# Kernel tuning notes

Measured on AMD Instinct MI355X. Metric: run time of the kernel, lower is better.

The kernel has to match this reference:

```python
import jax, jax.numpy as jnp
import numpy as np

B, T, C, H = 2, 2048, 1024, 16
D = C // H  # head dim = 64
EPS = 1e-5


def _layernorm(x, g, b):
    mu = jnp.mean(x, axis=-1, keepdims=True)
    var = jnp.mean((x - mu) ** 2, axis=-1, keepdims=True)
    return (x - mu) * jax.lax.rsqrt(var + EPS) * g + b


def setup_inputs() -> dict:
    key = jax.random.key(0)
    ks = jax.random.split(key, 16)
    s = 1.0 / np.sqrt(C)
    inp = {
        "x": jax.random.normal(ks[0], (B, T, C), dtype=jnp.float32),
        "Wq": jax.random.normal(ks[1], (C, C), dtype=jnp.float32) * s,
        "bq": jnp.zeros((C,), jnp.float32),
        "Wk": jax.random.normal(ks[2], (C, C), dtype=jnp.float32) * s,
        "bk": jnp.zeros((C,), jnp.float32),
        "Wv": jax.random.normal(ks[3], (C, C), dtype=jnp.float32) * s,
        "bv": jnp.zeros((C,), jnp.float32),
        "Wo": jax.random.normal(ks[4], (C, C), dtype=jnp.float32) * s,
        "bo": jnp.zeros((C,), jnp.float32),
        "ln1_g": jnp.ones((C,), jnp.float32),
        "ln1_b": jnp.zeros((C,), jnp.float32),
        "ln2_g": jnp.ones((C,), jnp.float32),
        "ln2_b": jnp.zeros((C,), jnp.float32),
        "W1": jax.random.normal(ks[5], (C, 4 * C), dtype=jnp.float32) * s,
        "b1": jnp.zeros((4 * C,), jnp.float32),
        "W2": jax.random.normal(ks[6], (4 * C, C), dtype=jnp.float32) * (1.0 / np.sqrt(4 * C)),
        "b2": jnp.zeros((C,), jnp.float32),
    }
    return inp


def _block(x, Wq, bq, Wk, bk, Wv, bv, Wo, bo, ln1_g, ln1_b, ln2_g, ln2_b, W1, b1, W2, b2):
    # --- attention sublayer (pre-LN, residual) ---
    h = _layernorm(x, ln1_g, ln1_b)
    q = (h @ Wq + bq).reshape(B, T, H, D)
    k = (h @ Wk + bk).reshape(B, T, H, D)
    v = (h @ Wv + bv).reshape(B, T, H, D)
    scores = jnp.einsum("bthd,bshd->bhts", q, k) * (1.0 / np.sqrt(D))
    attn = jax.nn.softmax(scores, axis=-1)  # dropout is identity at eval
    y = jnp.einsum("bhts,bshd->bthd", attn, v).reshape(B, T, C)
    x = x + (y @ Wo + bo)
    # --- MLP sublayer (pre-LN, residual) ---
    h2 = _layernorm(x, ln2_g, ln2_b)
    m = jax.nn.gelu(h2 @ W1 + b1, approximate=False)  # torch nn.GELU() is exact erf
    x = x + (m @ W2 + b2)
    return x


def reference(x, Wq, bq, Wk, bk, Wv, bv, Wo, bo, ln1_g, ln1_b, ln2_g, ln2_b, W1, b1, W2, b2):
    return _block(x, Wq, bq, Wk, bk, Wv, bv, Wo, bo, ln1_g, ln1_b, ln2_g, ln2_b, W1, b1, W2, b2)
```

## Files before the change

### kernel.cpp

```cpp
#include <hip/hip_runtime.h>
#include <math.h>

typedef unsigned short u16;
typedef unsigned int   u32;
using bf16x8 = __attribute__((ext_vector_type(8))) short;
using f32x4  = __attribute__((ext_vector_type(4))) float;
using f32x16 = __attribute__((ext_vector_type(16))) float;

static constexpr int Bb = 2, Tt = 2048, Cc = 1024, Hh = 16, Dd = 64;
static constexpr int QS = 3072;
static constexpr float QSCALE = 0.125f * 1.44269504089f;

__device__ __forceinline__ u16 f2bf(float f){
  u32 u = __builtin_bit_cast(u32, f);
  u += 0x7fffu + ((u >> 16) & 1u);
  return (u16)(u >> 16);
}
__device__ __forceinline__ float bf2f(u16 v){
  u32 u = (u32)v << 16;
  return __builtin_bit_cast(float, u);
}

__device__ __forceinline__ void gl2lds16(const void* g, void* l){
  __builtin_amdgcn_global_load_lds((const __attribute__((address_space(1))) void*)g,
                                   (__attribute__((address_space(3))) void*)l, 16, 0, 0);
}

template<int N> __device__ __forceinline__ void waitvm(){
  if constexpr (N == 0) asm volatile("s_waitcnt vmcnt(0)" ::: "memory");
  else if constexpr (N == 4) asm volatile("s_waitcnt vmcnt(4)" ::: "memory");
  else if constexpr (N == 6) asm volatile("s_waitcnt vmcnt(6)" ::: "memory");
  else if constexpr (N == 8) asm volatile("s_waitcnt vmcnt(8)" ::: "memory");
}

__device__ __forceinline__ void barrier_pin(){
  __builtin_amdgcn_s_barrier();
  __builtin_amdgcn_sched_barrier(0);
}

__device__ __forceinline__ f32x4 mfma16(bf16x8 a, bf16x8 b, f32x4 c){
  return __builtin_amdgcn_mfma_f32_16x16x32_bf16(a, b, c, 0, 0, 0);
}
__device__ __forceinline__ f32x16 mfma32(bf16x8 a, bf16x8 b, f32x16 c){
  return __builtin_amdgcn_mfma_f32_32x32x16_bf16(a, b, c, 0, 0, 0);
}

__device__ __forceinline__ float exp2f_fast(float x){
#if __has_builtin(__builtin_amdgcn_exp2f)
  return __builtin_amdgcn_exp2f(x);
#else
  return __expf(x * 0.69314718056f);
#endif
}

__device__ __forceinline__ float gelu_f(float x){
  return 0.5f * x * (1.0f + erff(x * 0.70710678118654752f));
}

__device__ __forceinline__ void plane_swap(u32& a, u32& b){
  asm("v_permlane32_swap_b32 %0, %1" : "+v"(a), "+v"(b));
}
__device__ __forceinline__ u32 cvtpk_bf16(float lo, float hi){
  u32 r;
  asm("v_cvt_pk_bf16_f32 %0, %1, %2" : "=v"(r) : "v"(lo), "v"(hi));
  return r;
}

__device__ __forceinline__ bf16x8 ldlds(const u16* p){ return *(const bf16x8*)p; }

__global__ __launch_bounds__(256) void ln_kernel(const float* __restrict__ x,
    const float* __restrict__ g, const float* __restrict__ b, u16* __restrict__ out)
{
  int row = blockIdx.x;
  int tid = threadIdx.x;
  const float4* xr = (const float4*)(x + (size_t)row * Cc);
  float4 v = xr[tid];
  float s  = v.x + v.y + v.z + v.w;
  float s2 = v.x*v.x + v.y*v.y + v.z*v.z + v.w*v.w;
  #pragma unroll
  for (int off = 1; off < 64; off <<= 1){ s += __shfl_xor(s, off); s2 += __shfl_xor(s2, off); }
  __shared__ float red[8];
  int wid = tid >> 6;
  if ((tid & 63) == 0){ red[wid] = s; red[4 + wid] = s2; }
  __syncthreads();
  s  = red[0] + red[1] + red[2] + red[3];
  s2 = red[4] + red[5] + red[6] + red[7];
  float mu   = s * (1.0f / Cc);
  float var  = s2 * (1.0f / Cc) - mu * mu;
  float rstd = rsqrtf(var + 1e-5f);
  const float4 gg = ((const float4*)g)[tid];
  const float4 bb = ((const float4*)b)[tid];
  ushort4 o;
  o.x = f2bf((v.x - mu) * rstd * gg.x + bb.x);
  o.y = f2bf((v.y - mu) * rstd * gg.y + bb.y);
  o.z = f2bf((v.z - mu) * rstd * gg.z + bb.z);
  o.w = f2bf((v.w - mu) * rstd * gg.w + bb.w);
  *(ushort4*)(out + (size_t)row * Cc + tid * 4) = o;
}

__global__ __launch_bounds__(256) void transpose_cast_kernel(const float* __restrict__ in,
    u16* __restrict__ out, int R, int Ccols)
{
  __shared__ float tile[32][33];
  int tx = threadIdx.x, ty = threadIdx.y;
  int c0 = blockIdx.x * 32, r0 = blockIdx.y * 32;
  #pragma unroll
  for (int j = 0; j < 4; j++) tile[ty + j*8][tx] = in[(size_t)(r0 + ty + j*8) * Ccols + c0 + tx];
  __syncthreads();
  #pragma unroll
  for (int j = 0; j < 4; j++) out[(size_t)(c0 + ty + j*8) * R + r0 + tx] = f2bf(tile[tx][ty + j*8]);
}

__global__ __launch_bounds__(256) void transpose4_kernel(
    const float* __restrict__ s0, const float* __restrict__ s1,
    const float* __restrict__ s2, const float* __restrict__ s3,
    u16* __restrict__ d0, u16* __restrict__ d1, u16* __restrict__ d2, u16* __restrict__ d3)
{
  __shared__ float tile[32][33];
  int z = blockIdx.z;
  const float* in = (z == 0) ? s0 : (z == 1) ? s1 : (z == 2) ? s2 : s3;
  u16* out        = (z == 0) ? d0 : (z == 1) ? d1 : (z == 2) ? d2 : d3;
  int tx = threadIdx.x, ty = threadIdx.y;
  int c0 = blockIdx.x * 32, r0 = blockIdx.y * 32;
  #pragma unroll
  for (int j = 0; j < 4; j++) tile[ty + j*8][tx] = in[(size_t)(r0 + ty + j*8) * 1024 + c0 + tx];
  __syncthreads();
  #pragma unroll
  for (int j = 0; j < 4; j++) out[(size_t)(c0 + ty + j*8) * 1024 + r0 + tx] = f2bf(tile[tx][ty + j*8]);
}

__global__ __launch_bounds__(256) void pack3_kernel(const float* __restrict__ a,
    const float* __restrict__ b, const float* __restrict__ c, float* __restrict__ o)
{
  int i = blockIdx.x * 256 + threadIdx.x;
  float v = (i < 1024) ? a[i] : (i < 2048 ? b[i - 1024] : c[i - 2048]);
  o[i] = v;
}

__global__ __launch_bounds__(256) void transpose_v_kernel(const u16* __restrict__ v, u16* __restrict__ vt)
{
  __shared__ u16 tile[32][33];
  int tx = threadIdx.x, ty = threadIdx.y;
  int bh = blockIdx.z; int b = bh >> 4, h = bh & 15;
  int t0 = blockIdx.x * 32, d0 = blockIdx.y * 32;
  const u16* src = v + (size_t)b * Tt * QS + h * Dd;
  #pragma unroll
  for (int j = 0; j < 4; j++) tile[ty + j*8][tx] = src[(size_t)(t0 + ty + j*8) * QS + d0 + tx];
  __syncthreads();
  u16* dst = vt + (size_t)bh * Dd * Tt;
  #pragma unroll
  for (int j = 0; j < 4; j++) dst[(size_t)(d0 + ty + j*8) * Tt + t0 + tx] = tile[tx][ty + j*8];
}

template<int BM, int BN, int WPEU, int EPI>
__global__ __launch_bounds__(256, WPEU) void gemmc_kernel(
    const u16* __restrict__ A, const u16* __restrict__ BT,
    const float* __restrict__ bias, const float* __restrict__ resid,
    void* __restrict__ out, int K, int ldA, int ldOut)
{
  constexpr int MF = BM / 2 / 16;
  constexpr int NF = BN / 2 / 16;
  constexpr int AG = BM / 32;
  constexpr int BG = BN / 32;
  constexpr int NLOADS = AG + BG;

  __shared__ alignas(16) u16 As[2][BM * 64];
  __shared__ alignas(16) u16 Bs[2][BN * 64];

  const int tid  = threadIdx.x;
  const int lane = tid & 63, wid = tid >> 6;
  const int l15  = lane & 15, lg = lane >> 4;

  const int gx  = gridDim.x;
  const int lin = blockIdx.x + gx * blockIdx.y;
  const int nwg = gx * gridDim.y;
  const int wl  = (lin & 7) * (nwg >> 3) + (lin >> 3);
  const int rowBase = (wl % gx) * BM, colBase = (wl / gx) * BN;

  const int wr = wid >> 1, wc = wid & 1;

  f32x4 acc[MF][NF] = {};

  const u16* pA[AG];
  const u16* pB[BG];
  u32 dA[AG], dB[BG];
  #pragma unroll
  for (int j = 0; j < AG; j++){
    int g = tid + 256 * j;
    int r = g >> 3, w = (g & 7) ^ (r & 7);
    pA[j] = A + (size_t)(rowBase + r) * ldA + w * 8;
    dA[j] = (u32)g * 8;
  }
  #pragma unroll
  for (int j = 0; j < BG; j++){
    int g = tid + 256 * j;
    int r = g >> 3, w = (g & 7) ^ (r & 7);
    pB[j] = BT + (size_t)(colBase + r) * K + w * 8;
    dB[j] = (u32)g * 8;
  }

  u32 oa[MF][2], ob[NF][2];
  #pragma unroll
  for (int mi = 0; mi < MF; mi++){
    int r = wr * (BM / 2) + mi * 16 + l15;
    oa[mi][0] = (u32)(r * 64 + ((lg       ^ (r & 7)) << 3));
    oa[mi][1] = (u32)(r * 64 + (((4 + lg) ^ (r & 7)) << 3));
  }
  #pragma unroll
  for (int ni = 0; ni < NF; ni++){
    int r = wc * (BN / 2) + ni * 16 + l15;
    ob[ni][0] = (u32)(r * 64 + ((lg       ^ (r & 7)) << 3));
    ob[ni][1] = (u32)(r * 64 + (((4 + lg) ^ (r & 7)) << 3));
  }

  #pragma unroll
  for (int j = 0; j < AG; j++){ gl2lds16(pA[j], &As[0][dA[j]]); pA[j] += 64; }
  #pragma unroll
  for (int j = 0; j < BG; j++){ gl2lds16(pB[j], &Bs[0][dB[j]]); pB[j] += 64; }

  const int nt = K >> 6;
  #pragma unroll 2
  for (int t = 0; t < nt - 1; ++t){
    const int cur = t & 1, nxt = cur ^ 1;
    #pragma unroll
    for (int j = 0; j < AG; j++){ gl2lds16(pA[j], &As[nxt][dA[j]]); pA[j] += 64; }
    #pragma unroll
    for (int j = 0; j < BG; j++){ gl2lds16(pB[j], &Bs[nxt][dB[j]]); pB[j] += 64; }
    waitvm<NLOADS>();
    __builtin_amdgcn_s_barrier();
    __builtin_amdgcn_sched_barrier(0);

    bf16x8 afr[MF][2], bfr[NF][2];
    #pragma unroll
    for (int mi = 0; mi < MF; mi++){
      afr[mi][0] = ldlds(&As[cur][oa[mi][0]]);
      afr[mi][1] = ldlds(&As[cur][oa[mi][1]]);
    }
    #pragma unroll
    for (int ni = 0; ni < NF; ni++){
      bfr[ni][0] = ldlds(&Bs[cur][ob[ni][0]]);
      bfr[ni][1] = ldlds(&Bs[cur][ob[ni][1]]);
    }
    __builtin_amdgcn_s_setprio(1);
    #pragma unroll
    for (int mi = 0; mi < MF; mi++)
      #pragma unroll
      for (int ni = 0; ni < NF; ni++){
        acc[mi][ni] = mfma16(afr[mi][0], bfr[ni][0], acc[mi][ni]);
        acc[mi][ni] = mfma16(afr[mi][1], bfr[ni][1], acc[mi][ni]);
      }
    __builtin_amdgcn_s_setprio(0);

    __builtin_amdgcn_sched_barrier(0);
    __builtin_amdgcn_s_barrier();
  }
  {
    const int cur = (nt - 1) & 1;
    waitvm<0>();
    __builtin_amdgcn_s_barrier();
    bf16x8 afr[MF][2], bfr[NF][2];
    #pragma unroll
    for (int mi = 0; mi < MF; mi++){
      afr[mi][0] = ldlds(&As[cur][oa[mi][0]]);
      afr[mi][1] = ldlds(&As[cur][oa[mi][1]]);
    }
    #pragma unroll
    for (int ni = 0; ni < NF; ni++){
      bfr[ni][0] = ldlds(&Bs[cur][ob[ni][0]]);
      bfr[ni][1] = ldlds(&Bs[cur][ob[ni][1]]);
    }
    #pragma unroll
    for (int mi = 0; mi < MF; mi++)
      #pragma unroll
      for (int ni = 0; ni < NF; ni++){
        acc[mi][ni] = mfma16(afr[mi][0], bfr[ni][0], acc[mi][ni]);
        acc[mi][ni] = mfma16(afr[mi][1], bfr[ni][1], acc[mi][ni]);
      }
  }

  #pragma unroll
  for (int mi = 0; mi < MF; mi++){
    #pragma unroll
    for (int ni = 0; ni < NF; ni++){
      int row = rowBase + wr * (BM / 2) + mi * 16 + lg * 4;
      int col = colBase + wc * (BN / 2) + ni * 16 + l15;
      float bc = bias[col];
      #pragma unroll
      for (int r = 0; r < 4; r++){
        float val = acc[mi][ni][r] + bc;
        size_t idx = (size_t)(row + r) * ldOut + col;
        if constexpr (EPI == 1)      ((float*)out)[idx] = val + resid[idx];
        else if constexpr (EPI == 2) ((u16*)out)[idx]   = f2bf(gelu_f(val));
        else if constexpr (EPI == 3) ((u16*)out)[idx]   = f2bf(col < 1024 ? val * QSCALE : val);
        else                         ((u16*)out)[idx]   = f2bf(val);
      }
    }
  }
}

__global__ __launch_bounds__(256, 4) void attn_kernel(const u16* __restrict__ q, const u16* __restrict__ k,
    const u16* __restrict__ vt, u16* __restrict__ opart, float* __restrict__ ml)
{
  __shared__ alignas(16) u16 Ks[2][64 * 64];
  __shared__ alignas(16) u16 Vs[2][64 * 64];
  int tid  = threadIdx.x;
  int lane = tid & 63, wid = tid >> 6;
  int l31  = lane & 31, hi = lane >> 5;

  int lin = blockIdx.x + 16 * blockIdx.y;
  int wl  = (lin & 7) * 64 + (lin >> 3);
  int qt  = wl & 15, bh = wl >> 4;
  int b = bh >> 4, h = bh & 15;
  int split = blockIdx.z;
  int kt0 = split * (Tt / 2);

  int qglob = qt * 128 + wid * 32 + l31;

  const u16* qp = q + ((size_t)b * Tt + qglob) * QS + h * Dd + hi * 8;
  bf16x8 qf[4];
  #pragma unroll
  for (int s = 0; s < 4; s++) qf[s] = *(const bf16x8*)(qp + s * 16);

  const u16* kbase = k  + (size_t)b * Tt * QS + h * Dd;
  const u16* vbase = vt + (size_t)bh * Dd * Tt;

  f32x16 yacc[2] = {};
  float m2 = -1e30f, lsum = 0.f;

  int g0 = tid, g1 = tid + 256;
  int r0 = g0 >> 3, cb0 = (g0 & 7) ^ (r0 & 7);
  int r1 = g1 >> 3, cb1 = (g1 & 7) ^ (r1 & 7);

  auto stageKV = [&](int buf, int kt){
    gl2lds16(kbase + (size_t)(kt + r0) * QS + cb0 * 8, (u16*)Ks[buf] + wid * 512);
    gl2lds16(kbase + (size_t)(kt + r1) * QS + cb1 * 8, (u16*)Ks[buf] + 2048 + wid * 512);
    gl2lds16(vbase + (size_t)r0 * Tt + kt + cb0 * 8,   (u16*)Vs[buf] + wid * 512);
    gl2lds16(vbase + (size_t)r1 * Tt + kt + cb1 * 8,   (u16*)Vs[buf] + 2048 + wid * 512);
  };

  stageKV(0, kt0);
  int cur = 0;
  for (int kt = kt0; kt < kt0 + Tt / 2; kt += 64) {
    if (kt + 64 < kt0 + Tt / 2) { stageKV(cur ^ 1, kt + 64); waitvm<4>(); }
    else                        { waitvm<0>(); }
    barrier_pin();

    const u16* Ksb = (const u16*)Ks[cur];
    const u16* Vsb = (const u16*)Vs[cur];
    int rx = l31 & 7;

    f32x16 st[2] = {};
    __builtin_amdgcn_s_setprio(1);
    #pragma unroll
    for (int nb = 0; nb < 2; nb++){
      const u16* krow = Ksb + (nb * 32 + l31) * 64;
      #pragma unroll
      for (int s = 0; s < 4; s++){
        bf16x8 kf = *(const bf16x8*)(krow + (((s * 2 + hi) ^ rx) << 3));
        st[nb] = mfma32(kf, qf[s], st[nb]);
      }
    }
    __builtin_amdgcn_s_setprio(0);

    float tm[16];
    #pragma unroll
    for (int i = 0; i < 16; i++) tm[i] = fmaxf(st[0][i], st[1][i]);
    #pragma unroll
    for (int w = 8; w; w >>= 1)
      #pragma unroll
      for (int i = 0; i < w; i++) tm[i] = fmaxf(tm[i], tm[i + w]);
    u32 ma = __builtin_bit_cast(u32, tm[0]), mb = ma;
    plane_swap(ma, mb);
    float mx = fmaxf(__builtin_bit_cast(float, ma), __builtin_bit_cast(float, mb));

    float mnew = fmaxf(m2, mx);
    float alpha = exp2f_fast(m2 - mnew);
    m2 = mnew;

    #pragma unroll
    for (int nb = 0; nb < 2; nb++)
      #pragma unroll
      for (int i = 0; i < 16; i++)
        st[nb][i] = exp2f_fast(st[nb][i] - m2);

    float ts[16];
    #pragma unroll
    for (int i = 0; i < 16; i++) ts[i] = st[0][i] + st[1][i];
    #pragma unroll
    for (int w = 8; w; w >>= 1)
      #pragma unroll
      for (int i = 0; i < w; i++) ts[i] += ts[i + w];
    u32 sa = __builtin_bit_cast(u32, ts[0]), sb = sa;
    plane_swap(sa, sb);
    lsum = lsum * alpha + __builtin_bit_cast(float, sa) + __builtin_bit_cast(float, sb);

    #pragma unroll
    for (int nd = 0; nd < 2; nd++)
      #pragma unroll
      for (int i = 0; i < 16; i++) yacc[nd][i] *= alpha;

    bf16x8 pb[4];
    #pragma unroll
    for (int nb = 0; nb < 2; nb++){
      u32 c[8];
      #pragma unroll
      for (int i = 0; i < 8; i++) c[i] = cvtpk_bf16(st[nb][2 * i], st[nb][2 * i + 1]);
      plane_swap(c[0], c[2]); plane_swap(c[1], c[3]);
      plane_swap(c[4], c[6]); plane_swap(c[5], c[7]);
      u32 f0[4] = {c[0], c[1], c[2], c[3]};
      u32 f1[4] = {c[4], c[5], c[6], c[7]};
      pb[nb * 2 + 0] = *(bf16x8*)f0;
      pb[nb * 2 + 1] = *(bf16x8*)f1;
    }

    __builtin_amdgcn_s_setprio(1);
    #pragma unroll
    for (int nd = 0; nd < 2; nd++){
      const u16* vrow = Vsb + (nd * 32 + l31) * 64;
      #pragma unroll
      for (int ks = 0; ks < 4; ks++){
        bf16x8 vf = *(const bf16x8*)(vrow + (((ks * 2 + hi) ^ rx) << 3));
        yacc[nd] = mfma32(vf, pb[ks], yacc[nd]);
      }
    }
    __builtin_amdgcn_s_setprio(0);

    __builtin_amdgcn_sched_barrier(0);
    barrier_pin();
    cur ^= 1;
  }

  float inv = 1.0f / lsum;
  u16* op = opart + ((size_t)split * (Bb * Tt) + (size_t)b * Tt + qglob) * Cc + h * Dd;
  #pragma unroll
  for (int nd = 0; nd < 2; nd++){
    #pragma unroll
    for (int g = 0; g < 4; g++){
      ushort4 o;
      o.x = f2bf(yacc[nd][g * 4 + 0] * inv);
      o.y = f2bf(yacc[nd][g * 4 + 1] * inv);
      o.z = f2bf(yacc[nd][g * 4 + 2] * inv);
      o.w = f2bf(yacc[nd][g * 4 + 3] * inv);
      *(ushort4*)(op + nd * 32 + g * 8 + hi * 4) = o;
    }
  }
  if (hi == 0){
    float* mlp = ml + (((size_t)split * (Bb * Tt) + (size_t)b * Tt + qglob) * Hh + h) * 2;
    mlp[0] = m2; mlp[1] = lsum;
  }
}

__global__ __launch_bounds__(256) void combine_kernel(const u16* __restrict__ opart,
    const float* __restrict__ ml, u16* __restrict__ y)
{
  int row = blockIdx.x;
  int d0  = threadIdx.x * 4;
  int h   = d0 >> 6;
  const float* p0 = ml + ((size_t)row * Hh + h) * 2;
  const float* p1 = ml + (((size_t)(Bb * Tt) + row) * Hh + h) * 2;
  float m0 = p0[0], l0 = p0[1], m1 = p1[0], l1 = p1[1];
  float M  = fmaxf(m0, m1);
  float u0 = l0 * exp2f_fast(m0 - M), u1 = l1 * exp2f_fast(m1 - M);
  float inv = 1.0f / (u0 + u1);
  float w0 = u0 * inv, w1 = u1 * inv;
  ushort4 a = *(const ushort4*)(opart + (size_t)row * Cc + d0);
  ushort4 c = *(const ushort4*)(opart + ((size_t)(Bb * Tt) + row) * Cc + d0);
  ushort4 o;
  o.x = f2bf(bf2f(a.x) * w0 + bf2f(c.x) * w1);
  o.y = f2bf(bf2f(a.y) * w0 + bf2f(c.y) * w1);
  o.z = f2bf(bf2f(a.z) * w0 + bf2f(c.z) * w1);
  o.w = f2bf(bf2f(a.w) * w0 + bf2f(c.w) * w1);
  *(ushort4*)(y + (size_t)row * Cc + d0) = o;
}

extern "C" void kernel_launch(void* const* d_in, const int* in_sizes, int n_in,
                              void* d_out, int out_size, void* d_ws, size_t ws_size,
                              hipStream_t stream)
{
  (void)in_sizes; (void)n_in; (void)out_size; (void)ws_size;
  const float* x    = (const float*)d_in[0];
  const float* Wq   = (const float*)d_in[1];
  const float* bq   = (const float*)d_in[2];
  const float* Wk   = (const float*)d_in[3];
  const float* bk   = (const float*)d_in[4];
  const float* Wv   = (const float*)d_in[5];
  const float* bv   = (const float*)d_in[6];
  const float* Wo   = (const float*)d_in[7];
  const float* bo   = (const float*)d_in[8];
  const float* ln1g = (const float*)d_in[9];
  const float* ln1b = (const float*)d_in[10];
  const float* ln2g = (const float*)d_in[11];
  const float* ln2b = (const float*)d_in[12];
  const float* W1   = (const float*)d_in[13];
  const float* b1   = (const float*)d_in[14];
  const float* W2   = (const float*)d_in[15];
  const float* b2   = (const float*)d_in[16];

  char* ws = (char*)d_ws;
  const size_t MB = 1024 * 1024;
  u16*   wqkvt = (u16*)(ws + 0 * MB);
  u16*   wot   = (u16*)(ws + 6 * MB);
  u16*   w1t   = (u16*)(ws + 8 * MB);
  u16*   w2t   = (u16*)(ws + 16 * MB);
  float* bqkv  = (float*)(ws + 24 * MB);
  u16*   hbuf  = (u16*)(ws + 25 * MB);
  u16*   qkv   = (u16*)(ws + 33 * MB);
  u16*   vtb   = (u16*)(ws + 57 * MB);
  u16*   yb    = (u16*)(ws + 65 * MB);
  u16*   opart = (u16*)(ws + 73 * MB);
  float* x2    = (float*)(ws + 73 * MB);
  float* mlb   = (float*)(ws + 89 * MB);
  u16*   h2    = hbuf;
  u16*   mb    = qkv;

  dim3 tb(32, 8);
  transpose4_kernel<<<dim3(32, 32, 4), tb, 0, stream>>>(Wq, Wk, Wv, Wo,
      wqkvt, wqkvt + 1024 * 1024, wqkvt + 2048 * 1024, wot);
  transpose_cast_kernel<<<dim3(128, 32), tb, 0, stream>>>(W1, w1t, 1024, 4096);
  transpose_cast_kernel<<<dim3(32, 128), tb, 0, stream>>>(W2, w2t, 4096, 1024);
  pack3_kernel<<<12, 256, 0, stream>>>(bq, bk, bv, bqkv);

  ln_kernel<<<4096, 256, 0, stream>>>(x, ln1g, ln1b, hbuf);

  gemmc_kernel<64, 128, 3, 3><<<dim3(64, 24), 256, 0, stream>>>(hbuf, wqkvt, bqkv, nullptr, qkv, 1024, 1024, 3072);

  transpose_v_kernel<<<dim3(64, 2, 32), tb, 0, stream>>>(qkv + 2048, vtb);

  attn_kernel<<<dim3(16, 32, 2), 256, 0, stream>>>(qkv, qkv + 1024, vtb, opart, mlb);
  combine_kernel<<<4096, 256, 0, stream>>>(opart, mlb, yb);

  gemmc_kernel<64, 64, 4, 1><<<dim3(64, 16), 256, 0, stream>>>(yb, wot, bo, x, x2, 1024, 1024, 1024);

  ln_kernel<<<4096, 256, 0, stream>>>(x2, ln2g, ln2b, h2);

  gemmc_kernel<64, 128, 3, 2><<<dim3(64, 32), 256, 0, stream>>>(h2, w1t, b1, nullptr, mb, 1024, 1024, 4096);

  gemmc_kernel<64, 64, 4, 1><<<dim3(64, 16), 256, 0, stream>>>(mb, w2t, b2, x2, (float*)d_out, 4096, 4096, 1024);
}
```

Before: 258.3 us.

## Add 256x256 eight-wave ping-pong GEMM for QKV and MLP-up projections

Adds a new 512-thread GEMM kernel with 256x256 output tiles, a split-K double-buffered LDS layout with XOR swizzle, and interleaved barriers and set-priority around MFMA phases. It replaces the smaller-tile kernel for the QKV and W1 projections. The W2 projection switches to a 128x64 tile configuration. Larger tiles cut global and LDS traffic per FLOP, at the cost of fewer workgroups (192 and 256) on a 256-CU part, which may leave CUs idle or unbalanced.

After: 250.4 us. -3.0%, faster.

```diff
diff --git a/kernel.cpp b/kernel.cpp
--- a/kernel.cpp
+++ b/kernel.cpp
@@ -152,6 +152,148 @@
   for (int j = 0; j < 4; j++) dst[(size_t)(d0 + ty + j*8) * Tt + t0 + tx] = tile[tx][ty + j*8];
 }
 
+template<int EPI, int KT>
+__global__ __launch_bounds__(512, 2) void gemm8p_kernel(
+    const u16* __restrict__ A, const u16* __restrict__ BT,
+    const float* __restrict__ bias, void* __restrict__ out,
+    int ldA, int ldOut)
+{
+  __shared__ alignas(16) u16 AsU[2][2][256 * 32];
+  __shared__ alignas(16) u16 BsU[2][2][256 * 32];
+
+  const int tid  = threadIdx.x;
+  const int lane = tid & 63, wid = tid >> 6;
+  const int l15  = lane & 15, lg = lane >> 4;
+
+  const int gx  = gridDim.x;
+  const int lin = blockIdx.x + gx * blockIdx.y;
+  const int nwg = gx * gridDim.y;
+  const int wl  = (lin & 7) * (nwg >> 3) + (lin >> 3);
+  const int rowBase = (wl % gx) * 256, colBase = (wl / gx) * 256;
+
+  const int wr = wid >> 2, wc = wid & 3;
+
+  f32x4 acc[8][4] = {};
+
+  const int s0 = tid, s1 = tid + 512;
+  const int r0 = s0 >> 2, w0 = (s0 & 3) ^ ((r0 >> 1) & 3);
+  const int r1 = s1 >> 2, w1 = (s1 & 3) ^ ((r1 >> 1) & 3);
+  const u16* pA0 = A  + (size_t)(rowBase + r0) * ldA + w0 * 8;
+  const u16* pA1 = A  + (size_t)(rowBase + r1) * ldA + w1 * 8;
+  const u16* pB0 = BT + (size_t)(colBase + r0) * KT  + w0 * 8;
+  const u16* pB1 = BT + (size_t)(colBase + r1) * KT  + w1 * 8;
+  const u32 d0 = (u32)s0 * 8, d1 = (u32)s1 * 8;
+
+#define AOFF8(pm, mi) ({ int r_ = wr*128 + (pm)*64 + (mi)*16 + l15; \
+                         (u32)(r_*32 + ((lg ^ ((r_>>1)&3)) << 3)); })
+#define BOFF8(ni)     ({ int r_ = wc*64 + (ni)*16 + l15; \
+                         (u32)(r_*32 + ((lg ^ ((r_>>1)&3)) << 3)); })
+  const u32 a00=AOFF8(0,0), a01=AOFF8(0,1), a02=AOFF8(0,2), a03=AOFF8(0,3);
+  const u32 a10=AOFF8(1,0), a11=AOFF8(1,1), a12=AOFF8(1,2), a13=AOFF8(1,3);
+  const u32 b0 =BOFF8(0),   b1 =BOFF8(1),   b2 =BOFF8(2),   b3 =BOFF8(3);
+#undef AOFF8
+#undef BOFF8
+
+  auto mfmaQ = [&](int pm, const bf16x8* a, const bf16x8* b){
+    __builtin_amdgcn_s_setprio(1);
+    #pragma unroll
+    for (int mi = 0; mi < 4; mi++)
+      #pragma unroll
+      for (int ni = 0; ni < 4; ni++)
+        acc[pm * 4 + mi][ni] = mfma16(a[mi], b[ni], acc[pm * 4 + mi][ni]);
+    __builtin_amdgcn_s_setprio(0);
+  };
+
+  gl2lds16(pA0,      &AsU[0][0][d0]); gl2lds16(pA1,      &AsU[0][0][d1]);
+  gl2lds16(pB0,      &BsU[0][0][d0]); gl2lds16(pB1,      &BsU[0][0][d1]);
+  gl2lds16(pA0 + 32, &AsU[0][1][d0]); gl2lds16(pA1 + 32, &AsU[0][1][d1]);
+  gl2lds16(pB0 + 32, &BsU[0][1][d0]); gl2lds16(pB1 + 32, &BsU[0][1][d1]);
+  pA0 += 64; pA1 += 64; pB0 += 64; pB1 += 64;
+  waitvm<4>();
+  __builtin_amdgcn_s_barrier();
+
+  constexpr int nt = KT >> 6;
+  bf16x8 a[4], b[4];
+  #pragma unroll 2
+  for (int t = 0; t < nt - 1; ++t){
+    const int cur = t & 1, nxt = cur ^ 1;
+    a[0]=ldlds(&AsU[cur][0][a00]); a[1]=ldlds(&AsU[cur][0][a01]);
+    a[2]=ldlds(&AsU[cur][0][a02]); a[3]=ldlds(&AsU[cur][0][a03]);
+    b[0]=ldlds(&BsU[cur][0][b0]);  b[1]=ldlds(&BsU[cur][0][b1]);
+    b[2]=ldlds(&BsU[cur][0][b2]);  b[3]=ldlds(&BsU[cur][0][b3]);
+    gl2lds16(pA0, &AsU[nxt][0][d0]); gl2lds16(pA1, &AsU[nxt][0][d1]);
+    __builtin_amdgcn_s_barrier();
+    mfmaQ(0, a, b);
+    __builtin_amdgcn_s_barrier();
+    a[0]=ldlds(&AsU[cur][0][a10]); a[1]=ldlds(&AsU[cur][0][a11]);
+    a[2]=ldlds(&AsU[cur][0][a12]); a[3]=ldlds(&AsU[cur][0][a13]);
+    gl2lds16(pB0, &BsU[nxt][0][d0]); gl2lds16(pB1, &BsU[nxt][0][d1]);
+    __builtin_amdgcn_s_barrier();
+    mfmaQ(1, a, b);
+    waitvm<4>();
+    __builtin_amdgcn_s_barrier();
+    a[0]=ldlds(&AsU[cur][1][a00]); a[1]=ldlds(&AsU[cur][1][a01]);
+    a[2]=ldlds(&AsU[cur][1][a02]); a[3]=ldlds(&AsU[cur][1][a03]);
+    b[0]=ldlds(&BsU[cur][1][b0]);  b[1]=ldlds(&BsU[cur][1][b1]);
+    b[2]=ldlds(&BsU[cur][1][b2]);  b[3]=ldlds(&BsU[cur][1][b3]);
+    gl2lds16(pA0 + 32, &AsU[nxt][1][d0]); gl2lds16(pA1 + 32, &AsU[nxt][1][d1]);
+    __builtin_amdgcn_s_barrier();
+    mfmaQ(0, a, b);
+    __builtin_amdgcn_s_barrier();
+    a[0]=ldlds(&AsU[cur][1][a10]); a[1]=ldlds(&AsU[cur][1][a11]);
+    a[2]=ldlds(&AsU[cur][1][a12]); a[3]=ldlds(&AsU[cur][1][a13]);
+    gl2lds16(pB0 + 32, &BsU[nxt][1][d0]); gl2lds16(pB1 + 32, &BsU[nxt][1][d1]);
+    __builtin_amdgcn_s_barrier();
+    mfmaQ(1, a, b);
+    waitvm<4>();
+    __builtin_amdgcn_s_barrier();
+    pA0 += 64; pA1 += 64; pB0 += 64; pB1 += 64;
+  }
+  {
+    const int cur = (nt - 1) & 1;
+    a[0]=ldlds(&AsU[cur][0][a00]); a[1]=ldlds(&AsU[cur][0][a01]);
+    a[2]=ldlds(&AsU[cur][0][a02]); a[3]=ldlds(&AsU[cur][0][a03]);
+    b[0]=ldlds(&BsU[cur][0][b0]);  b[1]=ldlds(&BsU[cur][0][b1]);
+    b[2]=ldlds(&BsU[cur][0][b2]);  b[3]=ldlds(&BsU[cur][0][b3]);
+    __builtin_amdgcn_s_barrier();
+    mfmaQ(0, a, b);
+    __builtin_amdgcn_s_barrier();
+    a[0]=ldlds(&AsU[cur][0][a10]); a[1]=ldlds(&AsU[cur][0][a11]);
+    a[2]=ldlds(&AsU[cur][0][a12]); a[3]=ldlds(&AsU[cur][0][a13]);
+    __builtin_amdgcn_s_barrier();
+    mfmaQ(1, a, b);
+    waitvm<0>();
+    __builtin_amdgcn_s_barrier();
+    a[0]=ldlds(&AsU[cur][1][a00]); a[1]=ldlds(&AsU[cur][1][a01]);
+    a[2]=ldlds(&AsU[cur][1][a02]); a[3]=ldlds(&AsU[cur][1][a03]);
+    b[0]=ldlds(&BsU[cur][1][b0]);  b[1]=ldlds(&BsU[cur][1][b1]);
+    b[2]=ldlds(&BsU[cur][1][b2]);  b[3]=ldlds(&BsU[cur][1][b3]);
+    __builtin_amdgcn_s_barrier();
+    mfmaQ(0, a, b);
+    __builtin_amdgcn_s_barrier();
+    a[0]=ldlds(&AsU[cur][1][a10]); a[1]=ldlds(&AsU[cur][1][a11]);
+    a[2]=ldlds(&AsU[cur][1][a12]); a[3]=ldlds(&AsU[cur][1][a13]);
+    mfmaQ(1, a, b);
+  }
+
+  #pragma unroll
+  for (int mi = 0; mi < 8; mi++){
+    #pragma unroll
+    for (int ni = 0; ni < 4; ni++){
+      int row = rowBase + wr * 128 + mi * 16 + lg * 4;
+      int col = colBase + wc * 64 + ni * 16 + l15;
+      float bc = bias[col];
+      #pragma unroll
+      for (int r = 0; r < 4; r++){
+        float val = acc[mi][ni][r] + bc;
+        size_t idx = (size_t)(row + r) * ldOut + col;
+        if constexpr (EPI == 2) ((u16*)out)[idx] = f2bf(gelu_f(val));
+        else                    ((u16*)out)[idx] = f2bf(col < 1024 ? val * QSCALE : val);
+      }
+    }
+  }
+}
+
 template<int BM, int BN, int WPEU, int EPI>
 __global__ __launch_bounds__(256, WPEU) void gemmc_kernel(
     const u16* __restrict__ A, const u16* __restrict__ BT,
@@ -289,10 +431,8 @@
       for (int r = 0; r < 4; r++){
         float val = acc[mi][ni][r] + bc;
         size_t idx = (size_t)(row + r) * ldOut + col;
-        if constexpr (EPI == 1)      ((float*)out)[idx] = val + resid[idx];
-        else if constexpr (EPI == 2) ((u16*)out)[idx]   = f2bf(gelu_f(val));
-        else if constexpr (EPI == 3) ((u16*)out)[idx]   = f2bf(col < 1024 ? val * QSCALE : val);
-        else                         ((u16*)out)[idx]   = f2bf(val);
+        if constexpr (EPI == 1) ((float*)out)[idx] = val + resid[idx];
+        else                    ((u16*)out)[idx]   = f2bf(val);
       }
     }
   }
@@ -522,7 +662,7 @@
 
   ln_kernel<<<4096, 256, 0, stream>>>(x, ln1g, ln1b, hbuf);
 
-  gemmc_kernel<64, 128, 3, 3><<<dim3(64, 24), 256, 0, stream>>>(hbuf, wqkvt, bqkv, nullptr, qkv, 1024, 1024, 3072);
+  gemm8p_kernel<3, 1024><<<dim3(16, 12), 512, 0, stream>>>(hbuf, wqkvt, bqkv, qkv, 1024, 3072);
 
   transpose_v_kernel<<<dim3(64, 2, 32), tb, 0, stream>>>(qkv + 2048, vtb);
 
@@ -533,7 +673,7 @@
 
   ln_kernel<<<4096, 256, 0, stream>>>(x2, ln2g, ln2b, h2);
 
-  gemmc_kernel<64, 128, 3, 2><<<dim3(64, 32), 256, 0, stream>>>(h2, w1t, b1, nullptr, mb, 1024, 1024, 4096);
-
-  gemmc_kernel<64, 64, 4, 1><<<dim3(64, 16), 256, 0, stream>>>(mb, w2t, b2, x2, (float*)d_out, 4096, 4096, 1024);
-}
+  gemm8p_kernel<2, 1024><<<dim3(16, 16), 512, 0, stream>>>(h2, w1t, b1, mb, 1024, 4096);
+
+  gemmc_kernel<128, 64, 3, 1><<<dim3(32, 16), 256, 0, stream>>>(mb, w2t, b2, x2, (float*)d_out, 4096, 4096, 1024);
+}
```

## Add 128x128-tile K32 GEMM kernel for QKV and MLP-up projections

Applied to the files above, without the earlier changes.

Introduces a new GEMM kernel with 128x128 output tiles, a K-step of 32 with a double-buffered LDS pipeline, an XOR-swizzled LDS layout and a workgroup remapping across the grid. The QKV projection and the W1+GELU projection now use it instead of the 64x128 generic kernel. Larger tiles give more operand reuse per LDS load and halve the workgroup count. The risks are fewer waves to fill the GPU and more barriers per unit of K. The old kernel's QKV and GELU epilogue branches are removed.

Result: slower. 455.9 us (+76.5%).

```diff
diff --git a/kernel.cpp b/kernel.cpp
--- a/kernel.cpp
+++ b/kernel.cpp
@@ -152,6 +152,115 @@
   for (int j = 0; j < 4; j++) dst[(size_t)(d0 + ty + j*8) * Tt + t0 + tx] = tile[tx][ty + j*8];
 }
 
+template<int EPI>
+__global__ __launch_bounds__(256, 5) void gemm32_kernel(
+    const u16* __restrict__ A, const u16* __restrict__ BT,
+    const float* __restrict__ bias, void* __restrict__ out,
+    int K, int ldA, int ldOut)
+{
+  __shared__ alignas(16) u16 As[2][128 * 32];
+  __shared__ alignas(16) u16 Bs[2][128 * 32];
+
+  const int tid  = threadIdx.x;
+  const int lane = tid & 63, wid = tid >> 6;
+  const int l15  = lane & 15, lg = lane >> 4;
+
+  const int gx  = gridDim.x;
+  const int lin = blockIdx.x + gx * blockIdx.y;
+  const int nwg = gx * gridDim.y;
+  const int wl  = (lin & 7) * (nwg >> 3) + (lin >> 3);
+  const int rowBase = (wl % gx) * 128, colBase = (wl / gx) * 128;
+
+  const int wr = wid >> 1, wc = wid & 1;
+
+  f32x4 acc[4][4] = {};
+
+  const int g0 = tid, g1 = tid + 256;
+  const int r0 = g0 >> 2, w0 = (g0 & 3) ^ ((r0 >> 1) & 3);
+  const int r1 = g1 >> 2, w1 = (g1 & 3) ^ ((r1 >> 1) & 3);
+  const u16* pA0 = A  + (size_t)(rowBase + r0) * ldA + w0 * 8;
+  const u16* pA1 = A  + (size_t)(rowBase + r1) * ldA + w1 * 8;
+  const u16* pB0 = BT + (size_t)(colBase + r0) * K   + w0 * 8;
+  const u16* pB1 = BT + (size_t)(colBase + r1) * K   + w1 * 8;
+  const u32 d0 = (u32)g0 * 8, d1 = (u32)g1 * 8;
+
+  u32 oa[4], ob[4];
+  #pragma unroll
+  for (int mi = 0; mi < 4; mi++){
+    int r = wr * 64 + mi * 16 + l15;
+    oa[mi] = (u32)(r * 32 + ((lg ^ ((r >> 1) & 3)) << 3));
+  }
+  #pragma unroll
+  for (int ni = 0; ni < 4; ni++){
+    int r = wc * 64 + ni * 16 + l15;
+    ob[ni] = (u32)(r * 32 + ((lg ^ ((r >> 1) & 3)) << 3));
+  }
+
+  gl2lds16(pA0, &As[0][d0]); gl2lds16(pA1, &As[0][d1]);
+  gl2lds16(pB0, &Bs[0][d0]); gl2lds16(pB1, &Bs[0][d1]);
+  pA0 += 32; pA1 += 32; pB0 += 32; pB1 += 32;
+
+  const int nt = K >> 5;
+  #pragma unroll 2
+  for (int t = 0; t < nt - 1; ++t){
+    const int cur = t & 1, nxt = cur ^ 1;
+    gl2lds16(pA0, &As[nxt][d0]); gl2lds16(pA1, &As[nxt][d1]);
+    gl2lds16(pB0, &Bs[nxt][d0]); gl2lds16(pB1, &Bs[nxt][d1]);
+    pA0 += 32; pA1 += 32; pB0 += 32; pB1 += 32;
+    waitvm<4>();
+    __builtin_amdgcn_s_barrier();
+    __builtin_amdgcn_sched_barrier(0);
+
+    bf16x8 afr[4], bfr[4];
+    #pragma unroll
+    for (int mi = 0; mi < 4; mi++) afr[mi] = ldlds(&As[cur][oa[mi]]);
+    #pragma unroll
+    for (int ni = 0; ni < 4; ni++) bfr[ni] = ldlds(&Bs[cur][ob[ni]]);
+    __builtin_amdgcn_s_setprio(1);
+    #pragma unroll
+    for (int mi = 0; mi < 4; mi++)
+      #pragma unroll
+      for (int ni = 0; ni < 4; ni++)
+        acc[mi][ni] = mfma16(afr[mi], bfr[ni], acc[mi][ni]);
+    __builtin_amdgcn_s_setprio(0);
+
+    __builtin_amdgcn_sched_barrier(0);
+    __builtin_amdgcn_s_barrier();
+  }
+  {
+    const int cur = (nt - 1) & 1;
+    waitvm<0>();
+    __builtin_amdgcn_s_barrier();
+    bf16x8 afr[4], bfr[4];
+    #pragma unroll
+    for (int mi = 0; mi < 4; mi++) afr[mi] = ldlds(&As[cur][oa[mi]]);
+    #pragma unroll
+    for (int ni = 0; ni < 4; ni++) bfr[ni] = ldlds(&Bs[cur][ob[ni]]);
+    #pragma unroll
+    for (int mi = 0; mi < 4; mi++)
+      #pragma unroll
+      for (int ni = 0; ni < 4; ni++)
+        acc[mi][ni] = mfma16(afr[mi], bfr[ni], acc[mi][ni]);
+  }
+
+  #pragma unroll
+  for (int mi = 0; mi < 4; mi++){
+    #pragma unroll
+    for (int ni = 0; ni < 4; ni++){
+      int row = rowBase + wr * 64 + mi * 16 + lg * 4;
+      int col = colBase + wc * 64 + ni * 16 + l15;
+      float bc = bias[col];
+      #pragma unroll
+      for (int r = 0; r < 4; r++){
+        float val = acc[mi][ni][r] + bc;
+        size_t idx = (size_t)(row + r) * ldOut + col;
+        if constexpr (EPI == 2) ((u16*)out)[idx] = f2bf(gelu_f(val));
+        else                    ((u16*)out)[idx] = f2bf(col < 1024 ? val * QSCALE : val);
+      }
+    }
+  }
+}
+
 template<int BM, int BN, int WPEU, int EPI>
 __global__ __launch_bounds__(256, WPEU) void gemmc_kernel(
     const u16* __restrict__ A, const u16* __restrict__ BT,
@@ -289,10 +398,8 @@
       for (int r = 0; r < 4; r++){
         float val = acc[mi][ni][r] + bc;
         size_t idx = (size_t)(row + r) * ldOut + col;
-        if constexpr (EPI == 1)      ((float*)out)[idx] = val + resid[idx];
-        else if constexpr (EPI == 2) ((u16*)out)[idx]   = f2bf(gelu_f(val));
-        else if constexpr (EPI == 3) ((u16*)out)[idx]   = f2bf(col < 1024 ? val * QSCALE : val);
-        else                         ((u16*)out)[idx]   = f2bf(val);
+        if constexpr (EPI == 1) ((float*)out)[idx] = val + resid[idx];
+        else                    ((u16*)out)[idx]   = f2bf(val);
       }
     }
   }
@@ -522,7 +629,7 @@
 
   ln_kernel<<<4096, 256, 0, stream>>>(x, ln1g, ln1b, hbuf);
 
-  gemmc_kernel<64, 128, 3, 3><<<dim3(64, 24), 256, 0, stream>>>(hbuf, wqkvt, bqkv, nullptr, qkv, 1024, 1024, 3072);
+  gemm32_kernel<3><<<dim3(32, 24), 256, 0, stream>>>(hbuf, wqkvt, bqkv, qkv, 1024, 1024, 3072);
 
   transpose_v_kernel<<<dim3(64, 2, 32), tb, 0, stream>>>(qkv + 2048, vtb);
 
@@ -533,7 +640,7 @@
 
   ln_kernel<<<4096, 256, 0, stream>>>(x2, ln2g, ln2b, h2);
 
-  gemmc_kernel<64, 128, 3, 2><<<dim3(64, 32), 256, 0, stream>>>(h2, w1t, b1, nullptr, mb, 1024, 1024, 4096);
+  gemm32_kernel<2><<<dim3(32, 32), 256, 0, stream>>>(h2, w1t, b1, mb, 1024, 1024, 4096);
 
   gemmc_kernel<64, 64, 4, 1><<<dim3(64, 16), 256, 0, stream>>>(mb, w2t, b2, x2, (float*)d_out, 4096, 4096, 1024);
 }
```
